# Optimization experiments

Measured on AMD Instinct MI355X. Metric: run time of the kernel, lower is better.

## Reference

```python
import jax, jax.numpy as jnp
import numpy as np

NEG_SLOPE = 0.01

def lrelu(x):
    return jax.nn.leaky_relu(x, NEG_SLOPE)

def lin(x, w, b):
    # torch Linear: x @ W.T + b, W shape (out, in)
    return x @ w.T + b

def meansum_pool(mask, x_local, *x_global):
    # masked sum + mean over points, concat with global/context vectors
    x_sum = (x_local * mask).sum(axis=1)                 # (b, d)
    x_mean = x_sum / mask.sum(axis=1)                    # (b, d) / (b, 1)
    return jnp.concatenate([x_mean, x_sum, *x_global], axis=1)


def setup_inputs() -> dict:
    key = jax.random.key(0)
    ks = jax.random.split(key, 16)
    B, N, DIN, DC, H, G, NB, DOUT = 16, 8192, 3, 16, 128, 10, 6, 3

    def w(k, shape, fan_in):
        return (jax.random.normal(k, shape, jnp.float32) / np.float32(np.sqrt(fan_in)))

    inp = {
        "x_local": jax.random.normal(ks[0], (B, N, DIN), jnp.float32),
        "context": jax.random.normal(ks[1], (B, DC), jnp.float32),
        "mask": (jax.random.uniform(ks[2], (B, N, 1)) < 0.9).astype(jnp.float32),
        # EPiC_Projection params (effective weight-normed weights)
        "proj_lw": w(ks[3], (H, DIN), DIN), "proj_lb": jnp.zeros((H,), jnp.float32),
        "proj_g0w": w(ks[4], (H, 2 * H + DC), 2 * H + DC), "proj_g0b": jnp.zeros((H,), jnp.float32),
        "proj_g1w": w(ks[5], (H, H), H), "proj_g1b": jnp.zeros((H,), jnp.float32),
        "proj_g2w": w(ks[6], (G, H), H), "proj_g2b": jnp.zeros((G,), jnp.float32),
        # stacked per-block EPiC_layer params
        "g1w": w(ks[7], (NB, H, 2 * H + G + DC), 2 * H + G + DC), "g1b": jnp.zeros((NB, H), jnp.float32),
        "g2w": w(ks[8], (NB, G, H), H), "g2b": jnp.zeros((NB, G), jnp.float32),
        "l1w": w(ks[9], (NB, H, H + G + DC), H + G + DC), "l1b": jnp.zeros((NB, H), jnp.float32),
        "l2w": w(ks[10], (NB, H, H), H), "l2b": jnp.zeros((NB, H), jnp.float32),
        # output head
        "outw": w(ks[11], (DOUT, H), H), "outb": jnp.zeros((DOUT,), jnp.float32),
    }
    return inp


def reference(x_local, context, mask,
              proj_lw, proj_lb, proj_g0w, proj_g0b, proj_g1w, proj_g1b, proj_g2w, proj_g2b,
              g1w, g1b, g2w, g2b, l1w, l1b, l2w, l2b, outw, outb):
    B, N, _ = x_local.shape
    # --- EPiC_Projection ---
    xl = lrelu(lin(x_local, proj_lw, proj_lb))           # (b, n, H)
    xg = meansum_pool(mask, xl, context)                 # (b, 2H + DC)
    xg = lrelu(lin(xg, proj_g0w, proj_g0b))
    xg = lrelu(lin(xg, proj_g1w, proj_g1b))
    xg = lrelu(lin(xg, proj_g2w, proj_g2b))              # (b, G)
    xl = xl * mask
    # --- EPiC layers (no skip: use_skip_connection=False -> +0) ---
    num_blocks = g1w.shape[0]
    for i in range(num_blocks):
        pooled = meansum_pool(mask, xl, xg, context)     # (b, 2H + G + DC)
        h_g = lrelu(lin(pooled, g1w[i], g1b[i]))
        xg = lrelu(lin(h_g, g2w[i], g2b[i]) + xg)        # residual global
        xg_b = jnp.broadcast_to(xg[:, None, :], (B, N, xg.shape[-1]))
        ctx_b = jnp.broadcast_to(context[:, None, :], (B, N, context.shape[-1]))
        cat = jnp.concatenate([xl, xg_b, ctx_b], axis=2)  # (b, n, H + G + DC)
        h_l = lrelu(lin(cat, l1w[i], l1b[i]))
        xl = lrelu(lin(h_l, l2w[i], l2b[i]) + xl) * mask  # residual local, masked
    h = lin(xl, outw, outb)                              # (b, n, 3)
    return h * mask
```

## Files before the change

kernel.cpp:

```cpp
#include <hip/hip_runtime.h>
#include <hip/hip_bf16.h>


typedef __attribute__((ext_vector_type(8))) short short8;
typedef __attribute__((ext_vector_type(4))) float f32x4;

#define B_ 16
#define N_ 8192
#define DC_ 16
#define H_ 128
#define G_ 10
#define NB_ 6
#define NEG_ 0.01f

__device__ __forceinline__ float lrelu(float x) { return x > 0.f ? x : NEG_ * x; }

__device__ __forceinline__ unsigned short f2bf(float x) {
  union { float f; unsigned u; } v; v.f = x;
  return (unsigned short)((v.u + 0x7fffu + ((v.u >> 16) & 1u)) >> 16);
}
__device__ __forceinline__ float bf2f(unsigned short u) {
  union { unsigned u; float f; } v; v.u = ((unsigned)u) << 16; return v.f;
}
__device__ __forceinline__ void split_bf(float x, unsigned short& h, unsigned short& l) {
  union { float f; unsigned u; } v; v.f = x;
  unsigned hu = v.u & 0xffff0000u;
  h = (unsigned short)(hu >> 16);
  union { unsigned u; float f; } hv; hv.u = hu;
  l = f2bf(x - hv.f);
}

__device__ __forceinline__ f32x4 mfma16(short8 a, short8 b, f32x4 c) {
  return __builtin_amdgcn_mfma_f32_16x16x32_bf16(a, b, c, 0, 0, 0);
}

__device__ __forceinline__ void make_frags(f32x4 v0, f32x4 v1, short8& bh, short8& bl) {
  unsigned short h, l;
#pragma unroll
  for (int j = 0; j < 4; ++j) {
    split_bf(v0[j], h, l);
    bh[j] = (short)h; bl[j] = (short)l;
  }
#pragma unroll
  for (int j = 0; j < 4; ++j) {
    split_bf(v1[j], h, l);
    bh[4 + j] = (short)h; bl[4 + j] = (short)l;
  }
}

__device__ __forceinline__ void async_cp16(const void* g, void* l) {
  __builtin_amdgcn_global_load_lds(
      (const __attribute__((address_space(1))) void*)g,
      (__attribute__((address_space(3))) void*)l, 16, 0, 0);
}

__device__ __forceinline__ void agent_store(float* p, float v) {
  __hip_atomic_store(p, v, __ATOMIC_RELAXED, __HIP_MEMORY_SCOPE_AGENT);
}
__device__ __forceinline__ float agent_load(const float* p) {
  return __hip_atomic_load(p, __ATOMIC_RELAXED, __HIP_MEMORY_SCOPE_AGENT);
}

template <int NS>
__device__ void epic_global_tail(
    int b, int tid, const float* __restrict__ pP, float cnt,
    const float* __restrict__ xg_cur, float* __restrict__ xg_next,
    const float* __restrict__ context,
    const float* __restrict__ g1w_n, const float* __restrict__ g1b_n,
    const float* __restrict__ g2w_n, const float* __restrict__ g2b_n,
    const float* __restrict__ l1w_n, const float* __restrict__ l1b_n,
    float* __restrict__ gbias_out, float* shx) {
  if (tid < 256) {
    const int f = tid & 127, kh = tid >> 7;
    const float* pr = pP + ((size_t)b * NS + kh * (NS / 2)) * 128 + f;
    float s = 0.f;
#pragma unroll 8
    for (int w = 0; w < NS / 2; ++w) s += agent_load(pr + w * 128);
    shx[tid] = s;
  }
  __syncthreads();
  if (tid < 128) {
    float s = shx[tid] + shx[tid + 128];
    shx[384 + tid] = s;
    shx[256 + tid] = s / cnt;
  }
  if (tid < G_) shx[512 + tid] = xg_cur[tid];
  if (tid >= 32 && tid < 32 + DC_) shx[522 + tid - 32] = context[b * DC_ + tid - 32];
  __syncthreads();
  if (tid < 256) {
    const int f = tid & 127, kh = tid >> 7;
    const float* wr = g1w_n + (size_t)f * 282 + kh * 142;
    const float* vp = shx + 256 + kh * 142;
    const int n2 = kh ? 70 : 71;
    float a = 0.f;
#pragma unroll 8
    for (int j = 0; j < n2; ++j) {
      float2 w2 = *(const float2*)(wr + 2 * j);
      a += w2.x * vp[2 * j] + w2.y * vp[2 * j + 1];
    }
    shx[tid] = a;
  }
  __syncthreads();
  if (tid < 128) shx[544 + tid] = lrelu(shx[tid] + shx[tid + 128] + g1b_n[tid]);
  __syncthreads();
  if (tid < G_) {
    const float* wr = g2w_n + tid * 128;
    float a = g2b_n[tid] + shx[512 + tid];
#pragma unroll 8
    for (int j = 0; j < 32; ++j) {
      float4 w4 = *(const float4*)(wr + 4 * j);
      a += w4.x * shx[544 + 4 * j] + w4.y * shx[544 + 4 * j + 1] +
           w4.z * shx[544 + 4 * j + 2] + w4.w * shx[544 + 4 * j + 3];
    }
    float v = lrelu(a);
    shx[672 + tid] = v;
    xg_next[tid] = v;
  }
  __syncthreads();
  if (tid < 128) {
    const float* wr = l1w_n + tid * 154;
    float a = l1b_n[tid];
#pragma unroll
    for (int j = 0; j < G_; ++j) a += wr[128 + j] * shx[672 + j];
#pragma unroll
    for (int j = 0; j < DC_; ++j) a += wr[138 + j] * shx[522 + j];
    gbias_out[tid] = a;
  }
}

__global__ __launch_bounds__(256) void prep_weights(
    const float* __restrict__ l1w, const float* __restrict__ l2w,
    unsigned short* __restrict__ w1h, unsigned short* __restrict__ w1l,
    unsigned short* __restrict__ w2h, unsigned short* __restrict__ w2l,
    unsigned int* __restrict__ counters) {
  int idx = blockIdx.x * 256 + threadIdx.x;
  const int total = NB_ * H_ * H_;
  if (idx < 112) counters[idx] = 0u;
  if (idx < total) {
    int i = idx / (H_ * H_), rem = idx % (H_ * H_);
    int F = rem / H_, k = rem % H_;
    int ks = k >> 5, c = k & 31;
    int mt2 = F >> 4, r2 = F & 15;
    int mt1 = ((F >> 5) << 1) | ((F >> 2) & 1);
    int r1 = (((F >> 3) & 3) << 2) | (F & 3);
    int off1 = i * 16384 + (mt1 * 4 + ks) * 512 + ((c >> 3) * 16 + r1) * 8 + (c & 7);
    int off2 = i * 16384 + (mt2 * 4 + ks) * 512 + ((c >> 3) * 16 + r2) * 8 + (c & 7);
    unsigned short h, l;
    split_bf(l1w[(i * H_ + F) * 154 + k], h, l);
    w1h[off1] = h; w1l[off1] = l;
    split_bf(l2w[(i * H_ + F) * H_ + k], h, l);
    w2h[off2] = h; w2l[off2] = l;
  }
}

__global__ __launch_bounds__(256, 2) void proj_local_kernel(
    const float* __restrict__ xloc, const float* __restrict__ maskp,
    const float* __restrict__ plw, const float* __restrict__ plb,
    float* __restrict__ xlf, float* __restrict__ pP,
    float* __restrict__ cntp, float* __restrict__ cnt_g,
    unsigned int* __restrict__ counters,
    const float* __restrict__ context,
    const float* __restrict__ g0w, const float* __restrict__ g0b,
    const float* __restrict__ g1pw, const float* __restrict__ g1pb,
    const float* __restrict__ g2pw, const float* __restrict__ g2pb,
    float* __restrict__ xg_g,
    const float* __restrict__ g1w0, const float* __restrict__ g1b0,
    const float* __restrict__ g2w0, const float* __restrict__ g2b0,
    const float* __restrict__ l1w0, const float* __restrict__ l1b0,
    float* __restrict__ gbias_g) {
  __shared__ float wq[H_][4];
  __shared__ float wsum[512];
  __shared__ float cw[4];
  __shared__ float shx[768];
  __shared__ int winflag;
  const int tid = threadIdx.x, bid = blockIdx.x;
  const int wv = tid >> 6, lane = tid & 63;
  const int q = lane >> 4, n16 = lane & 15;
  const int b = bid >> 6;
  if (tid < H_) {
    wq[tid][0] = plw[tid * 3 + 0];
    wq[tid][1] = plw[tid * 3 + 1];
    wq[tid][2] = plw[tid * 3 + 2];
    wq[tid][3] = plb[tid];
  }
  __syncthreads();
  const int t = bid * 4 + wv;
  const int p0 = t * 32;
  const int pa = p0 + n16, pb = p0 + 16 + n16;
  const float xa0 = xloc[pa * 3], xa1 = xloc[pa * 3 + 1], xa2 = xloc[pa * 3 + 2];
  const float xb0 = xloc[pb * 3], xb1 = xloc[pb * 3 + 1], xb2 = xloc[pb * 3 + 2];
  const float m0 = maskp[pa], m1 = maskp[pb];
  float* ga = xlf + (size_t)(2 * t) * 2048;
  float* gb = ga + 2048;
#pragma unroll
  for (int ms = 0; ms < 8; ++ms) {
    f32x4 v0, v1;
#pragma unroll
    for (int r = 0; r < 4; ++r) {
      const int F = ms * 16 + q * 4 + r;
      float4 w4 = *(const float4*)wq[F];
      v0[r] = lrelu(w4.x * xa0 + w4.y * xa1 + w4.z * xa2 + w4.w) * m0;
      v1[r] = lrelu(w4.x * xb0 + w4.y * xb1 + w4.z * xb2 + w4.w) * m1;
    }
    *(f32x4*)(ga + ms * 256 + (q * 16 + n16) * 4) = v0;
    *(f32x4*)(gb + ms * 256 + (q * 16 + n16) * 4) = v1;
    f32x4 s = v0 + v1;
#pragma unroll
    for (int r = 0; r < 4; ++r) {
      float sv = s[r];
      sv += __shfl_xor(sv, 1, 64);
      sv += __shfl_xor(sv, 2, 64);
      sv += __shfl_xor(sv, 4, 64);
      sv += __shfl_xor(sv, 8, 64);
      s[r] = sv;
    }
    if (n16 == 0) *(f32x4*)&wsum[wv * 128 + ms * 16 + q * 4] = s;
  }
  {
    float c = (q == 0) ? (m0 + m1) : 0.f;
    c += __shfl_xor(c, 1, 64);
    c += __shfl_xor(c, 2, 64);
    c += __shfl_xor(c, 4, 64);
    c += __shfl_xor(c, 8, 64);
    if (lane == 0) cw[wv] = c;
  }
  __syncthreads();
  if (tid < 128) {
    agent_store(&pP[(size_t)(2 * bid) * 128 + tid], wsum[tid] + wsum[128 + tid]);
    agent_store(&pP[(size_t)(2 * bid + 1) * 128 + tid], wsum[256 + tid] + wsum[384 + tid]);
  }
  if (tid == 0) agent_store(&cntp[bid], cw[0] + cw[1] + cw[2] + cw[3]);

  __syncthreads();
  if (tid == 0) winflag = (atomicAdd(&counters[b], 1u) == 63u) ? 1 : 0;
  __syncthreads();
  if (!winflag) return;
  if (tid < 64) shx[688 + tid] = agent_load(&cntp[b * 64 + tid]);
  __syncthreads();
  if (tid == 0) {
    float c = 0.f;
#pragma unroll
    for (int w = 0; w < 64; ++w) c += shx[688 + w];
    shx[752] = c;
    cnt_g[b] = c;
  }
  __syncthreads();
  const float cnt = shx[752];
  {
    const int f = tid & 127, kh = tid >> 7;
    const float* pr = pP + ((size_t)b * 128 + kh * 64) * 128 + f;
    float s = 0.f;
#pragma unroll 8
    for (int w = 0; w < 64; ++w) s += agent_load(pr + w * 128);
    shx[tid] = s;
  }
  __syncthreads();
  if (tid < 128) {
    float s = shx[tid] + shx[tid + 128];
    shx[384 + tid] = s;
    shx[256 + tid] = s / cnt;
  }
  if (tid < DC_) shx[512 + tid] = context[b * DC_ + tid];
  __syncthreads();
  {
    const int f = tid & 127, kh = tid >> 7;
    const float* wr = g0w + (size_t)f * 272 + kh * 136;
    const float* vp = shx + 256 + kh * 136;
    float a = 0.f;
#pragma unroll 8
    for (int j = 0; j < 34; ++j) {
      float4 w4 = *(const float4*)(wr + 4 * j);
      a += w4.x * vp[4 * j] + w4.y * vp[4 * j + 1] + w4.z * vp[4 * j + 2] + w4.w * vp[4 * j + 3];
    }
    __syncthreads();
    shx[tid] = a;
  }
  __syncthreads();
  if (tid < 128) shx[544 + tid] = lrelu(shx[tid] + shx[tid + 128] + g0b[tid]);
  __syncthreads();
  {
    const int f = tid & 127, kh = tid >> 7;
    const float* wr = g1pw + (size_t)f * 128 + kh * 64;
    const float* vp = shx + 544 + kh * 64;
    float a = 0.f;
#pragma unroll 8
    for (int j = 0; j < 16; ++j) {
      float4 w4 = *(const float4*)(wr + 4 * j);
      a += w4.x * vp[4 * j] + w4.y * vp[4 * j + 1] + w4.z * vp[4 * j + 2] + w4.w * vp[4 * j + 3];
    }
    __syncthreads();
    shx[tid] = a;
  }
  __syncthreads();
  if (tid < 128) shx[544 + tid] = lrelu(shx[tid] + shx[tid + 128] + g1pb[tid]);
  __syncthreads();
  if (tid < G_) {
    const float* wr = g2pw + tid * 128;
    float a = g2pb[tid];
#pragma unroll 8
    for (int j = 0; j < 32; ++j) {
      float4 w4 = *(const float4*)(wr + 4 * j);
      a += w4.x * shx[544 + 4 * j] + w4.y * shx[544 + 4 * j + 1] +
           w4.z * shx[544 + 4 * j + 2] + w4.w * shx[544 + 4 * j + 3];
    }
    xg_g[(0 * 16 + b) * 16 + tid] = lrelu(a);
  }
  __syncthreads();
  epic_global_tail<128>(b, tid, pP, cnt,
                        xg_g + (0 * 16 + b) * 16, xg_g + (1 * 16 + b) * 16, context,
                        g1w0, g1b0, g2w0, g2b0, l1w0, l1b0,
                        gbias_g + (size_t)(0 * 16 + b) * 128, shx);
}

template <bool LAST>
__global__ __launch_bounds__(1024) void epic_local_kernel(
    float* __restrict__ xlf, float* __restrict__ pP,
    const float* __restrict__ cnt_g, unsigned int* __restrict__ counters_blk,
    const float* __restrict__ gbias_in,
    const float* __restrict__ xg_tail_cur, float* __restrict__ xg_tail_next,
    float* __restrict__ gbias_tail_out,
    const float* __restrict__ context,
    const float* __restrict__ g1w_n, const float* __restrict__ g1b_n,
    const float* __restrict__ g2w_n, const float* __restrict__ g2b_n,
    const float* __restrict__ l1w_n, const float* __restrict__ l1b_n,
    const float* __restrict__ l2b,
    const unsigned short* __restrict__ w1h, const unsigned short* __restrict__ w1l,
    const unsigned short* __restrict__ w2h, const unsigned short* __restrict__ w2l,
    const float* __restrict__ maskp,
    const float* __restrict__ outw, const float* __restrict__ outb,
    float* __restrict__ outp) {
  __shared__ unsigned short wbuf[65536];
  __shared__ float shx[768];
  __shared__ float gbias_s[128];
  __shared__ float l2b_s[128];
  __shared__ float wsum[2048];
  __shared__ float outw_s[392];
  __shared__ int winflag;
  const int tid = threadIdx.x, bid = blockIdx.x;
  const int b = bid >> 5;
  const int wv = tid >> 6, lane = tid & 63;
  const int q = lane >> 4, n16 = lane & 15;

  {
    const unsigned short* src =
        (wv < 4) ? w1h : (wv < 8) ? w1l : (wv < 12) ? w2h : w2l;
    const char* s8 = (const char*)(src + (wv & 3) * 4096) + lane * 16;
    char* d8 = (char*)wbuf + wv * 8192;
#pragma unroll
    for (int j = 0; j < 8; ++j) async_cp16(s8 + j * 1024, d8 + j * 1024);
  }
  if (tid < 128) {
    gbias_s[tid] = gbias_in[b * 128 + tid];
    l2b_s[tid] = l2b[tid];
  }
  if (LAST) {
    if (tid < 384) outw_s[tid] = outw[tid];
    if (tid >= 384 && tid < 387) outw_s[tid] = outb[tid - 384];
  }

  const int g = bid * 16 + wv;
  const float* base_g = xlf + (size_t)g * 2048;
  short8 xbh[4], xbl[4];
#pragma unroll
  for (int ks = 0; ks < 4; ++ks) {
    const float* pb = base_g + (2 * ks + (q >> 1)) * 256 + ((q & 1) * 32 + n16) * 4;
    f32x4 v0 = *(const f32x4*)pb;
    f32x4 v1 = *(const f32x4*)(pb + 64);
    make_frags(v0, v1, xbh[ks], xbl[ks]);
  }
  __syncthreads();

  const unsigned short* w1h_l = wbuf;
  const unsigned short* w1l_l = wbuf + 16384;
  const unsigned short* w2h_l = wbuf + 32768;
  const unsigned short* w2l_l = wbuf + 49152;
  const int lane16 = lane * 8;

  f32x4 acc2[8];
#pragma unroll
  for (int ms = 0; ms < 8; ++ms) acc2[ms] = (f32x4){0.f, 0.f, 0.f, 0.f};

#pragma unroll 1
  for (int ko = 0; ko < 4; ++ko) {
    f32x4 acc[2];
    acc[0] = (f32x4){0.f, 0.f, 0.f, 0.f};
    acc[1] = (f32x4){0.f, 0.f, 0.f, 0.f};
#pragma unroll
    for (int t = 0; t < 2; ++t) {
#pragma unroll
      for (int kc = 0; kc < 2; ++kc) {
        short8 a1h[2], a1l[2];
#pragma unroll
        for (int u = 0; u < 2; ++u) {
          const int off = ((ko * 2 + t) * 4 + kc * 2 + u) * 512 + lane16;
          a1h[u] = *(const short8*)(w1h_l + off);
          a1l[u] = *(const short8*)(w1l_l + off);
        }
#pragma unroll
        for (int u = 0; u < 2; ++u) {
          const int ks = kc * 2 + u;
          acc[t] = mfma16(a1h[u], xbh[ks], acc[t]);
          acc[t] = mfma16(a1l[u], xbh[ks], acc[t]);
          acc[t] = mfma16(a1h[u], xbl[ks], acc[t]);
        }
      }
    }
    f32x4 gb0 = *(const f32x4*)&gbias_s[ko * 32 + q * 8];
    f32x4 gb1 = *(const f32x4*)&gbias_s[ko * 32 + q * 8 + 4];
    f32x4 hv0, hv1;
#pragma unroll
    for (int r = 0; r < 4; ++r) {
      hv0[r] = lrelu(acc[0][r] + gb0[r]);
      hv1[r] = lrelu(acc[1][r] + gb1[r]);
    }
    short8 b2h, b2l;
    make_frags(hv0, hv1, b2h, b2l);
#pragma unroll
    for (int mc = 0; mc < 4; ++mc) {
      short8 a2h[2], a2l[2];
#pragma unroll
      for (int u = 0; u < 2; ++u) {
        const int off = ((mc * 2 + u) * 4 + ko) * 512 + lane16;
        a2h[u] = *(const short8*)(w2h_l + off);
        a2l[u] = *(const short8*)(w2l_l + off);
      }
#pragma unroll
      for (int u = 0; u < 2; ++u) {
        const int ms = mc * 2 + u;
        acc2[ms] = mfma16(a2h[u], b2h, acc2[ms]);
        acc2[ms] = mfma16(a2l[u], b2h, acc2[ms]);
        acc2[ms] = mfma16(a2h[u], b2l, acc2[ms]);
      }
    }
  }

  const float mk = maskp[g * 16 + n16];
  f32x4 vsum[8];
  float po[3];
  if (!LAST) {
#pragma unroll
    for (int ms = 0; ms < 8; ++ms) vsum[ms] = (f32x4){0.f, 0.f, 0.f, 0.f};
  } else {
    po[0] = po[1] = po[2] = 0.f;
  }
  float* base_w = xlf + (size_t)g * 2048;
#pragma unroll
  for (int ms = 0; ms < 8; ++ms) {
    f32x4 lb4 = *(const f32x4*)&l2b_s[ms * 16 + q * 4];
    float* xo = base_w + ms * 256 + (q * 16 + n16) * 4;
    f32x4 old = *(const f32x4*)xo;
    f32x4 v;
#pragma unroll
    for (int r = 0; r < 4; ++r) v[r] = lrelu(acc2[ms][r] + lb4[r] + old[r]) * mk;
    if (!LAST) {
      *(f32x4*)xo = v;
      vsum[ms] += v;
    } else {
      f32x4 w0 = *(const f32x4*)&outw_s[0 * 128 + ms * 16 + q * 4];
      f32x4 w1 = *(const f32x4*)&outw_s[1 * 128 + ms * 16 + q * 4];
      f32x4 w2 = *(const f32x4*)&outw_s[2 * 128 + ms * 16 + q * 4];
#pragma unroll
      for (int r = 0; r < 4; ++r) {
        po[0] += v[r] * w0[r];
        po[1] += v[r] * w1[r];
        po[2] += v[r] * w2[r];
      }
    }
  }
  if (LAST) {
#pragma unroll
    for (int o = 0; o < 3; ++o) {
      float s = po[o];
      s += __shfl_xor(s, 16, 64);
      s += __shfl_xor(s, 32, 64);
      po[o] = s;
    }
    if (q == 0) {
      const int p = g * 16 + n16;
#pragma unroll
      for (int o = 0; o < 3; ++o)
        outp[(size_t)p * 3 + o] = (po[o] + outw_s[384 + o]) * mk;
    }
    return;
  }
#pragma unroll
  for (int ms = 0; ms < 8; ++ms) {
    f32x4 sr;
#pragma unroll
    for (int r = 0; r < 4; ++r) {
      float s = vsum[ms][r];
      s += __shfl_xor(s, 1, 64);
      s += __shfl_xor(s, 2, 64);
      s += __shfl_xor(s, 4, 64);
      s += __shfl_xor(s, 8, 64);
      sr[r] = s;
    }
    if (n16 == 0) *(f32x4*)&wsum[wv * 128 + ms * 16 + q * 4] = sr;
  }
  __syncthreads();
  if (tid < 128) {
    float s = 0.f;
#pragma unroll
    for (int w = 0; w < 16; ++w) s += wsum[w * 128 + tid];
    agent_store(&pP[(size_t)bid * 128 + tid], s);
  }

  __syncthreads();
  if (tid == 0) winflag = (atomicAdd(&counters_blk[b], 1u) == 31u) ? 1 : 0;
  __syncthreads();
  if (!winflag) return;
  epic_global_tail<32>(b, tid, pP, cnt_g[b], xg_tail_cur + b * 16, xg_tail_next + b * 16,
                       context, g1w_n, g1b_n, g2w_n, g2b_n, l1w_n, l1b_n,
                       gbias_tail_out + (size_t)b * 128, shx);
}

extern "C" void kernel_launch(void* const* d_in, const int* in_sizes, int n_in,
                              void* d_out, int out_size, void* d_ws, size_t ws_size,
                              hipStream_t stream) {
  const float* x_local = (const float*)d_in[0];
  const float* context = (const float*)d_in[1];
  const float* mask = (const float*)d_in[2];
  const float* proj_lw = (const float*)d_in[3];
  const float* proj_lb = (const float*)d_in[4];
  const float* proj_g0w = (const float*)d_in[5];
  const float* proj_g0b = (const float*)d_in[6];
  const float* proj_g1w = (const float*)d_in[7];
  const float* proj_g1b = (const float*)d_in[8];
  const float* proj_g2w = (const float*)d_in[9];
  const float* proj_g2b = (const float*)d_in[10];
  const float* g1w = (const float*)d_in[11];
  const float* g1b = (const float*)d_in[12];
  const float* g2w = (const float*)d_in[13];
  const float* g2b = (const float*)d_in[14];
  const float* l1w = (const float*)d_in[15];
  const float* l1b = (const float*)d_in[16];
  const float* l2w = (const float*)d_in[17];
  const float* l2b = (const float*)d_in[18];
  const float* outw = (const float*)d_in[19];
  const float* outb = (const float*)d_in[20];
  float* out = (float*)d_out;

  char* ws = (char*)d_ws;
  float* xlf = (float*)ws;
  float* pP = (float*)(ws + 67108864);
  float* cntp = (float*)(ws + 68157440);
  float* cnt_g = (float*)(ws + 68161536);
  float* xg_g = (float*)(ws + 68161600);
  float* gbias_g = (float*)(ws + 68168768);
  unsigned int* counters = (unsigned int*)(ws + 68217920);
  unsigned short* w1h = (unsigned short*)(ws + 68218368);
  unsigned short* w1l = (unsigned short*)(ws + 68414976);
  unsigned short* w2h = (unsigned short*)(ws + 68611584);
  unsigned short* w2l = (unsigned short*)(ws + 68808192);

  prep_weights<<<384, 256, 0, stream>>>(l1w, l2w, w1h, w1l, w2h, w2l, counters);
  proj_local_kernel<<<1024, 256, 0, stream>>>(
      x_local, mask, proj_lw, proj_lb, xlf, pP, cntp, cnt_g, counters, context,
      proj_g0w, proj_g0b, proj_g1w, proj_g1b, proj_g2w, proj_g2b, xg_g,
      g1w, g1b, g2w, g2b, l1w, l1b, gbias_g);
  for (int i = 0; i < NB_; ++i) {
    const int j = i + 1;
    const float* g1w_n = g1w + (size_t)j * 128 * 282;
    const float* g1b_n = g1b + j * 128;
    const float* g2w_n = g2w + j * 10 * 128;
    const float* g2b_n = g2b + j * 10;
    const float* l1w_n = l1w + (size_t)j * 128 * 154;
    const float* l1b_n = l1b + j * 128;
    const unsigned short* w1h_i = w1h + i * 16384;
    const unsigned short* w1l_i = w1l + i * 16384;
    const unsigned short* w2h_i = w2h + i * 16384;
    const unsigned short* w2l_i = w2l + i * 16384;
    if (i == NB_ - 1) {
      epic_local_kernel<true><<<512, 1024, 0, stream>>>(
          xlf, pP, cnt_g, counters + (i + 1) * 16, gbias_g + (size_t)(i * 16) * 128,
          nullptr, nullptr, nullptr, context,
          nullptr, nullptr, nullptr, nullptr, nullptr, nullptr,
          l2b + i * 128, w1h_i, w1l_i, w2h_i, w2l_i, mask, outw, outb, out);
    } else {
      epic_local_kernel<false><<<512, 1024, 0, stream>>>(
          xlf, pP, cnt_g, counters + (i + 1) * 16, gbias_g + (size_t)(i * 16) * 128,
          xg_g + (i + 1) * 16 * 16, xg_g + (i + 2) * 16 * 16,
          gbias_g + (size_t)((i + 1) * 16) * 128, context,
          g1w_n, g1b_n, g2w_n, g2b_n, l1w_n, l1b_n,
          l2b + i * 128, w1h_i, w1l_i, w2h_i, w2l_i, mask, outw, outb, out);
    }
  }
}
```

Measured before the change: 492.3 us.

## Process two point tiles per block to amortize LDS weight staging

Halves the grid of each EPiC local kernel so every block handles two 256-point groups in sequence. The 128 KB of split-bf16 weights is staged into LDS once and reused for both groups, and the global tail's completion counter threshold is adjusted to match. The first GEMM now keeps two independent accumulator chains per output tile to shorten MFMA dependency chains, and the wave-level column sums are reduced inside the epilogue instead of being held in registers. The cost is fewer blocks in flight (256 on a 256-CU part), extra barriers between the two passes, and less latency hiding per CU.

```diff
diff --git a/kernel.cpp b/kernel.cpp
--- a/kernel.cpp
+++ b/kernel.cpp
@@ -312,6 +312,140 @@
                         gbias_g + (size_t)(0 * 16 + b) * 128, shx);
 }
 
+__device__ __forceinline__ void load_frags(const float* base_g, int q, int n16,
+                                           short8* xbh, short8* xbl) {
+#pragma unroll
+  for (int ks = 0; ks < 4; ++ks) {
+    const float* pb = base_g + (2 * ks + (q >> 1)) * 256 + ((q & 1) * 32 + n16) * 4;
+    f32x4 v0 = *(const f32x4*)pb;
+    f32x4 v1 = *(const f32x4*)(pb + 64);
+    make_frags(v0, v1, xbh[ks], xbl[ks]);
+  }
+}
+
+template <bool LAST>
+__device__ __forceinline__ void epic_pass(
+    int g, int wv, int q, int n16, int lane16,
+    const short8* xbh, const short8* xbl,
+    const unsigned short* w1h_l, const unsigned short* w1l_l,
+    const unsigned short* w2h_l, const unsigned short* w2l_l,
+    const float* gbias_s, const float* l2b_s, const float* outw_s,
+    float* wsum, float* __restrict__ xlf, const float* __restrict__ maskp,
+    float* __restrict__ outp) {
+  f32x4 acc2[8];
+#pragma unroll
+  for (int ms = 0; ms < 8; ++ms) acc2[ms] = (f32x4){0.f, 0.f, 0.f, 0.f};
+
+#pragma unroll 1
+  for (int ko = 0; ko < 4; ++ko) {
+    f32x4 acc[2][2];
+#pragma unroll
+    for (int t = 0; t < 2; ++t)
+#pragma unroll
+      for (int kc = 0; kc < 2; ++kc) acc[t][kc] = (f32x4){0.f, 0.f, 0.f, 0.f};
+#pragma unroll
+    for (int t = 0; t < 2; ++t) {
+#pragma unroll
+      for (int kc = 0; kc < 2; ++kc) {
+        short8 a1h[2], a1l[2];
+#pragma unroll
+        for (int u = 0; u < 2; ++u) {
+          const int off = ((ko * 2 + t) * 4 + kc * 2 + u) * 512 + lane16;
+          a1h[u] = *(const short8*)(w1h_l + off);
+          a1l[u] = *(const short8*)(w1l_l + off);
+        }
+#pragma unroll
+        for (int u = 0; u < 2; ++u) {
+          const int ks = kc * 2 + u;
+          acc[t][kc] = mfma16(a1h[u], xbh[ks], acc[t][kc]);
+          acc[t][kc] = mfma16(a1l[u], xbh[ks], acc[t][kc]);
+          acc[t][kc] = mfma16(a1h[u], xbl[ks], acc[t][kc]);
+        }
+      }
+    }
+    f32x4 gb0 = *(const f32x4*)&gbias_s[ko * 32 + q * 8];
+    f32x4 gb1 = *(const f32x4*)&gbias_s[ko * 32 + q * 8 + 4];
+    f32x4 hv0, hv1;
+#pragma unroll
+    for (int r = 0; r < 4; ++r) {
+      hv0[r] = lrelu(acc[0][0][r] + acc[0][1][r] + gb0[r]);
+      hv1[r] = lrelu(acc[1][0][r] + acc[1][1][r] + gb1[r]);
+    }
+    short8 b2h, b2l;
+    make_frags(hv0, hv1, b2h, b2l);
+#pragma unroll
+    for (int mc = 0; mc < 4; ++mc) {
+      short8 a2h[2], a2l[2];
+#pragma unroll
+      for (int u = 0; u < 2; ++u) {
+        const int off = ((mc * 2 + u) * 4 + ko) * 512 + lane16;
+        a2h[u] = *(const short8*)(w2h_l + off);
+        a2l[u] = *(const short8*)(w2l_l + off);
+      }
+#pragma unroll
+      for (int u = 0; u < 2; ++u) {
+        const int ms = mc * 2 + u;
+        acc2[ms] = mfma16(a2h[u], b2h, acc2[ms]);
+        acc2[ms] = mfma16(a2l[u], b2h, acc2[ms]);
+        acc2[ms] = mfma16(a2h[u], b2l, acc2[ms]);
+      }
+    }
+  }
+
+  const float mk = maskp[g * 16 + n16];
+  float po[3];
+  if (LAST) po[0] = po[1] = po[2] = 0.f;
+  float* base_w = xlf + (size_t)g * 2048;
+#pragma unroll
+  for (int ms = 0; ms < 8; ++ms) {
+    f32x4 lb4 = *(const f32x4*)&l2b_s[ms * 16 + q * 4];
+    float* xo = base_w + ms * 256 + (q * 16 + n16) * 4;
+    f32x4 old = *(const f32x4*)xo;
+    f32x4 v;
+#pragma unroll
+    for (int r = 0; r < 4; ++r) v[r] = lrelu(acc2[ms][r] + lb4[r] + old[r]) * mk;
+    if (!LAST) {
+      *(f32x4*)xo = v;
+      f32x4 sr;
+#pragma unroll
+      for (int r = 0; r < 4; ++r) {
+        float s = v[r];
+        s += __shfl_xor(s, 1, 64);
+        s += __shfl_xor(s, 2, 64);
+        s += __shfl_xor(s, 4, 64);
+        s += __shfl_xor(s, 8, 64);
+        sr[r] = s;
+      }
+      if (n16 == 0) *(f32x4*)&wsum[wv * 128 + ms * 16 + q * 4] = sr;
+    } else {
+      f32x4 w0 = *(const f32x4*)&outw_s[0 * 128 + ms * 16 + q * 4];
+      f32x4 w1 = *(const f32x4*)&outw_s[1 * 128 + ms * 16 + q * 4];
+      f32x4 w2 = *(const f32x4*)&outw_s[2 * 128 + ms * 16 + q * 4];
+#pragma unroll
+      for (int r = 0; r < 4; ++r) {
+        po[0] += v[r] * w0[r];
+        po[1] += v[r] * w1[r];
+        po[2] += v[r] * w2[r];
+      }
+    }
+  }
+  if (LAST) {
+#pragma unroll
+    for (int o = 0; o < 3; ++o) {
+      float s = po[o];
+      s += __shfl_xor(s, 16, 64);
+      s += __shfl_xor(s, 32, 64);
+      po[o] = s;
+    }
+    if (q == 0) {
+      const int p = g * 16 + n16;
+#pragma unroll
+      for (int o = 0; o < 3; ++o)
+        outp[(size_t)p * 3 + o] = (po[o] + outw_s[384 + o]) * mk;
+    }
+  }
+}
+
 template <bool LAST>
 __global__ __launch_bounds__(1024) void epic_local_kernel(
     float* __restrict__ xlf, float* __restrict__ pP,
@@ -337,7 +471,8 @@
   __shared__ float outw_s[392];
   __shared__ int winflag;
   const int tid = threadIdx.x, bid = blockIdx.x;
-  const int b = bid >> 5;
+  const int b = bid >> 4;
+  const int wb = bid & 15;
   const int wv = tid >> 6, lane = tid & 63;
   const int q = lane >> 4, n16 = lane & 15;
 
@@ -358,16 +493,10 @@
     if (tid >= 384 && tid < 387) outw_s[tid] = outb[tid - 384];
   }
 
-  const int g = bid * 16 + wv;
-  const float* base_g = xlf + (size_t)g * 2048;
+  const int gA = bid * 32 + wv;
+  const int gB = bid * 32 + 16 + wv;
   short8 xbh[4], xbl[4];
-#pragma unroll
-  for (int ks = 0; ks < 4; ++ks) {
-    const float* pb = base_g + (2 * ks + (q >> 1)) * 256 + ((q & 1) * 32 + n16) * 4;
-    f32x4 v0 = *(const f32x4*)pb;
-    f32x4 v1 = *(const f32x4*)(pb + 64);
-    make_frags(v0, v1, xbh[ks], xbl[ks]);
-  }
+  load_frags(xlf + (size_t)gA * 2048, q, n16, xbh, xbl);
   __syncthreads();
 
   const unsigned short* w1h_l = wbuf;
@@ -376,137 +505,33 @@
   const unsigned short* w2l_l = wbuf + 49152;
   const int lane16 = lane * 8;
 
-  f32x4 acc2[8];
-#pragma unroll
-  for (int ms = 0; ms < 8; ++ms) acc2[ms] = (f32x4){0.f, 0.f, 0.f, 0.f};
-
-#pragma unroll 1
-  for (int ko = 0; ko < 4; ++ko) {
-    f32x4 acc[2];
-    acc[0] = (f32x4){0.f, 0.f, 0.f, 0.f};
-    acc[1] = (f32x4){0.f, 0.f, 0.f, 0.f};
-#pragma unroll
-    for (int t = 0; t < 2; ++t) {
-#pragma unroll
-      for (int kc = 0; kc < 2; ++kc) {
-        short8 a1h[2], a1l[2];
-#pragma unroll
-        for (int u = 0; u < 2; ++u) {
-          const int off = ((ko * 2 + t) * 4 + kc * 2 + u) * 512 + lane16;
-          a1h[u] = *(const short8*)(w1h_l + off);
-          a1l[u] = *(const short8*)(w1l_l + off);
-        }
-#pragma unroll
-        for (int u = 0; u < 2; ++u) {
-          const int ks = kc * 2 + u;
-          acc[t] = mfma16(a1h[u], xbh[ks], acc[t]);
-          acc[t] = mfma16(a1l[u], xbh[ks], acc[t]);
-          acc[t] = mfma16(a1h[u], xbl[ks], acc[t]);
-        }
-      }
-    }
-    f32x4 gb0 = *(const f32x4*)&gbias_s[ko * 32 + q * 8];
-    f32x4 gb1 = *(const f32x4*)&gbias_s[ko * 32 + q * 8 + 4];
-    f32x4 hv0, hv1;
-#pragma unroll
-    for (int r = 0; r < 4; ++r) {
-      hv0[r] = lrelu(acc[0][r] + gb0[r]);
-      hv1[r] = lrelu(acc[1][r] + gb1[r]);
-    }
-    short8 b2h, b2l;
-    make_frags(hv0, hv1, b2h, b2l);
-#pragma unroll
-    for (int mc = 0; mc < 4; ++mc) {
-      short8 a2h[2], a2l[2];
-#pragma unroll
-      for (int u = 0; u < 2; ++u) {
-        const int off = ((mc * 2 + u) * 4 + ko) * 512 + lane16;
-        a2h[u] = *(const short8*)(w2h_l + off);
-        a2l[u] = *(const short8*)(w2l_l + off);
-      }
-#pragma unroll
-      for (int u = 0; u < 2; ++u) {
-        const int ms = mc * 2 + u;
-        acc2[ms] = mfma16(a2h[u], b2h, acc2[ms]);
-        acc2[ms] = mfma16(a2l[u], b2h, acc2[ms]);
-        acc2[ms] = mfma16(a2h[u], b2l, acc2[ms]);
-      }
-    }
-  }
-
-  const float mk = maskp[g * 16 + n16];
-  f32x4 vsum[8];
-  float po[3];
+  epic_pass<LAST>(gA, wv, q, n16, lane16, xbh, xbl, w1h_l, w1l_l, w2h_l, w2l_l,
+                  gbias_s, l2b_s, outw_s, wsum, xlf, maskp, outp);
   if (!LAST) {
-#pragma unroll
-    for (int ms = 0; ms < 8; ++ms) vsum[ms] = (f32x4){0.f, 0.f, 0.f, 0.f};
-  } else {
-    po[0] = po[1] = po[2] = 0.f;
-  }
-  float* base_w = xlf + (size_t)g * 2048;
-#pragma unroll
-  for (int ms = 0; ms < 8; ++ms) {
-    f32x4 lb4 = *(const f32x4*)&l2b_s[ms * 16 + q * 4];
-    float* xo = base_w + ms * 256 + (q * 16 + n16) * 4;
-    f32x4 old = *(const f32x4*)xo;
-    f32x4 v;
-#pragma unroll
-    for (int r = 0; r < 4; ++r) v[r] = lrelu(acc2[ms][r] + lb4[r] + old[r]) * mk;
-    if (!LAST) {
-      *(f32x4*)xo = v;
-      vsum[ms] += v;
-    } else {
-      f32x4 w0 = *(const f32x4*)&outw_s[0 * 128 + ms * 16 + q * 4];
-      f32x4 w1 = *(const f32x4*)&outw_s[1 * 128 + ms * 16 + q * 4];
-      f32x4 w2 = *(const f32x4*)&outw_s[2 * 128 + ms * 16 + q * 4];
-#pragma unroll
-      for (int r = 0; r < 4; ++r) {
-        po[0] += v[r] * w0[r];
-        po[1] += v[r] * w1[r];
-        po[2] += v[r] * w2[r];
-      }
-    }
-  }
-  if (LAST) {
-#pragma unroll
-    for (int o = 0; o < 3; ++o) {
-      float s = po[o];
-      s += __shfl_xor(s, 16, 64);
-      s += __shfl_xor(s, 32, 64);
-      po[o] = s;
-    }
-    if (q == 0) {
-      const int p = g * 16 + n16;
-#pragma unroll
-      for (int o = 0; o < 3; ++o)
-        outp[(size_t)p * 3 + o] = (po[o] + outw_s[384 + o]) * mk;
-    }
-    return;
-  }
-#pragma unroll
-  for (int ms = 0; ms < 8; ++ms) {
-    f32x4 sr;
-#pragma unroll
-    for (int r = 0; r < 4; ++r) {
-      float s = vsum[ms][r];
-      s += __shfl_xor(s, 1, 64);
-      s += __shfl_xor(s, 2, 64);
-      s += __shfl_xor(s, 4, 64);
-      s += __shfl_xor(s, 8, 64);
-      sr[r] = s;
-    }
-    if (n16 == 0) *(f32x4*)&wsum[wv * 128 + ms * 16 + q * 4] = sr;
-  }
+    __syncthreads();
+    if (tid < 128) {
+      float s = 0.f;
+#pragma unroll
+      for (int w = 0; w < 16; ++w) s += wsum[w * 128 + tid];
+      agent_store(&pP[(size_t)(bid * 2) * 128 + tid], s);
+    }
+    __syncthreads();
+  }
+
+  load_frags(xlf + (size_t)gB * 2048, q, n16, xbh, xbl);
+  epic_pass<LAST>(gB, wv, q, n16, lane16, xbh, xbl, w1h_l, w1l_l, w2h_l, w2l_l,
+                  gbias_s, l2b_s, outw_s, wsum, xlf, maskp, outp);
+  if (LAST) return;
   __syncthreads();
   if (tid < 128) {
     float s = 0.f;
 #pragma unroll
     for (int w = 0; w < 16; ++w) s += wsum[w * 128 + tid];
-    agent_store(&pP[(size_t)bid * 128 + tid], s);
-  }
-
-  __syncthreads();
-  if (tid == 0) winflag = (atomicAdd(&counters_blk[b], 1u) == 31u) ? 1 : 0;
+    agent_store(&pP[(size_t)(bid * 2 + 1) * 128 + tid], s);
+  }
+
+  __syncthreads();
+  if (tid == 0) winflag = (atomicAdd(&counters_blk[b], 1u) == 15u) ? 1 : 0;
   __syncthreads();
   if (!winflag) return;
   epic_global_tail<32>(b, tid, pP, cnt_g[b], xg_tail_cur + b * 16, xg_tail_next + b * 16,
@@ -571,13 +596,13 @@
     const unsigned short* w2h_i = w2h + i * 16384;
     const unsigned short* w2l_i = w2l + i * 16384;
     if (i == NB_ - 1) {
-      epic_local_kernel<true><<<512, 1024, 0, stream>>>(
+      epic_local_kernel<true><<<256, 1024, 0, stream>>>(
           xlf, pP, cnt_g, counters + (i + 1) * 16, gbias_g + (size_t)(i * 16) * 128,
           nullptr, nullptr, nullptr, context,
           nullptr, nullptr, nullptr, nullptr, nullptr, nullptr,
           l2b + i * 128, w1h_i, w1l_i, w2h_i, w2l_i, mask, outw, outb, out);
     } else {
-      epic_local_kernel<false><<<512, 1024, 0, stream>>>(
+      epic_local_kernel<false><<<256, 1024, 0, stream>>>(
           xlf, pP, cnt_g, counters + (i + 1) * 16, gbias_g + (size_t)(i * 16) * 128,
           xg_g + (i + 1) * 16 * 16, xg_g + (i + 2) * 16 * 16,
           gbias_g + (size_t)((i + 1) * 16) * 128, context,
```

After: 477.3 us. 1.03x faster.
